# Kernel optimization log

Measured on AMD Instinct MI355X. Metric: run time of the kernel, lower is better.

Reference implementation:

```python
import jax, jax.numpy as jnp
import numpy as np

K = 7          # kernel_size
G = 16         # group_number
C = 256        # channel
R = 4          # reduction_ratio
BN_EPS = 1e-3  # keras BatchNormalization default epsilon


def setup_inputs() -> dict:
    key = jax.random.key(0)
    ks = jax.random.split(key, 8)
    B, H, W = 2, 64, 64
    Cr = C // R
    x = jax.random.normal(ks[0], (B, H, W, C), dtype=jnp.float32)
    # kernel_gen params: 1x1 conv (C->C/r), BN, ReLU, 1x1 conv (C/r -> K*K*G)
    w1 = jax.random.normal(ks[1], (C, Cr), dtype=jnp.float32) * (1.0 / np.sqrt(C))
    b1 = jnp.zeros((Cr,), dtype=jnp.float32)
    gamma = jnp.ones((Cr,), dtype=jnp.float32) + 0.1 * jax.random.normal(ks[2], (Cr,), dtype=jnp.float32)
    beta = 0.1 * jax.random.normal(ks[3], (Cr,), dtype=jnp.float32)
    mu = 0.1 * jax.random.normal(ks[4], (Cr,), dtype=jnp.float32)
    var = jnp.ones((Cr,), dtype=jnp.float32) + 0.05 * jax.random.uniform(ks[5], (Cr,), dtype=jnp.float32)
    w2 = jax.random.normal(ks[6], (Cr, K * K * G), dtype=jnp.float32) * (1.0 / np.sqrt(Cr))
    b2 = jnp.zeros((K * K * G,), dtype=jnp.float32)
    return {"x": x, "w1": w1, "b1": b1, "gamma": gamma, "beta": beta,
            "mu": mu, "var": var, "w2": w2, "b2": b2}


def reference(x, w1, b1, gamma, beta, mu, var, w2, b2):
    B, H, W, _ = x.shape
    # stride == 1 -> stride_layer is identity; kernel_input = x
    # kernel_gen: 1x1 conv -> BN (inference) -> ReLU -> 1x1 conv
    t = jnp.einsum('bhwc,cd->bhwd', x, w1) + b1
    t = gamma * (t - mu) * jax.lax.rsqrt(var + BN_EPS) + beta
    t = jax.nn.relu(t)
    kern = jnp.einsum('bhwd,dk->bhwk', t, w2) + b2            # (B,H,W,K*K*G)
    kern = kern.reshape(B, H, W, K * K, 1, G)                  # (B,H,W,KK,1,G)
    # tf.image.extract_patches SAME, stride 1 -> pad K//2 each side, zeros
    pad = K // 2
    xp = jnp.pad(x, ((0, 0), (pad, pad), (pad, pad), (0, 0)))
    # patch layout matches TF: (kh, kw) outer, channel inner
    patches = jnp.stack(
        [xp[:, i:i + H, j:j + W, :] for i in range(K) for j in range(K)],
        axis=3)                                                # (B,H,W,KK,C)
    patches = patches.reshape(B, H, W, K * K, C // G, G)
    out = jnp.sum(kern * patches, axis=3)                      # (B,H,W,C/G,G)
    out = out.reshape(B, H, W, C)
    return out, kern
```

## Files before the change

### kernel.cpp

```cpp
#include <hip/hip_runtime.h>


typedef __attribute__((ext_vector_type(8))) short short8;
typedef __attribute__((ext_vector_type(4))) float f32x4;

#define OUT_ELEMS 2097152
#define W2S_OFF 0
#define W1S_OFF 131072
#define BNS_OFF (131072 + 32768)
#define BNH_OFF (BNS_OFF + 256)

static __device__ __forceinline__ ushort f2bf(float f) {
    union { float f; unsigned u; } v; v.f = f;
    return (ushort)((v.u + 0x7FFFu + ((v.u >> 16) & 1u)) >> 16);
}

__global__ __launch_bounds__(256)
void prep(const float* __restrict__ w1, const float* __restrict__ w2,
          const float* __restrict__ b1, const float* __restrict__ gamma_,
          const float* __restrict__ beta_, const float* __restrict__ mu_,
          const float* __restrict__ var_, char* __restrict__ base)
{
    const int g = blockIdx.x * 256 + threadIdx.x;
    ushort* w2s = (ushort*)(base + W2S_OFF);
    ushort* w1s = (ushort*)(base + W1S_OFF);
    float*  bns = (float*)(base + BNS_OFF);
    float*  bnh = (float*)(base + BNH_OFF);
    if (g < 50176) {
        const int e = g & 7, lane = (g >> 3) & 63, kgks = g >> 9;
        const int kg = kgks >> 1, ks = kgks & 1;
        const int n = kg * 16 + (lane & 15);
        const int k = ks * 32 + ((lane >> 4) << 3) + e;
        w2s[g] = f2bf(w2[k * 784 + n]);
    } else if (g < 66560) {
        const int e2 = g - 50176;
        const int e = e2 & 7, lane = (e2 >> 3) & 63, ntks = e2 >> 9;
        const int nt = ntks >> 3, ks = ntks & 7;
        const int n = nt * 16 + (lane & 15);
        const int k = ks * 32 + ((lane >> 4) << 3) + e;
        w1s[e2] = f2bf(w1[k * 64 + n]);
    } else if (g < 66624) {
        const int d = g - 66560;
        const float s = gamma_[d] * rsqrtf(var_[d] + 1e-3f);
        bns[d] = s;
        bnh[d] = beta_[d] + (b1[d] - mu_[d]) * s;
    }
}

#define FMA4(A, K, X) \
    A.x = fmaf(K.x, X.x, A.x); A.y = fmaf(K.y, X.y, A.y); \
    A.z = fmaf(K.z, X.z, A.z); A.w = fmaf(K.w, X.w, A.w);

__global__ __launch_bounds__(256)
void invol_fused(const float* __restrict__ x, const char* __restrict__ base,
                 const float* __restrict__ b2, float* __restrict__ kern_out,
                 float* __restrict__ out)
{
    __shared__ __align__(16) union {
        struct { ushort xb[2048]; ushort tb[1024]; } s;
        float kl[6272];
    } u;

    const ushort* w2s = (const ushort*)(base + W2S_OFF);
    const ushort* w1s = (const ushort*)(base + W1S_OFF);
    const float*  bns = (const float*)(base + BNS_OFF);
    const float*  bnh = (const float*)(base + BNH_OFF);

    const int tid  = threadIdx.x;
    const int lane = tid & 63;
    const int wv   = tid >> 6;
    const int bid  = blockIdx.x;
    const int pb   = ((bid & 7) << 10) + ((bid >> 3) << 3);
    const int b  = pb >> 12;
    const int h  = (pb >> 6) & 63;
    const int w0 = pb & 63;

#pragma unroll
    for (int i = 0; i < 2; ++i) {
        const int f4 = tid + 256 * i;
        const int px = f4 >> 6;
        const int c0 = (f4 & 63) * 4;
        const float4 v = *(const float4*)(x + (size_t)(pb + px) * 256 + c0);
        ushort4 hh;
        hh.x = f2bf(v.x); hh.y = f2bf(v.y); hh.z = f2bf(v.z); hh.w = f2bf(v.w);
        const int byte = ((px << 9) + (c0 << 1)) ^ ((px & 7) << 4);
        *(ushort4*)((char*)u.s.xb + byte) = hh;
    }
    __syncthreads();

    const int qlane = lane >> 4;
    const int mrow  = lane & 15;
    const int apx   = mrow & 7;
    const int aswz  = (apx & 7) << 4;

    f32x4 acc = {0.f, 0.f, 0.f, 0.f};
#pragma unroll
    for (int ks = 0; ks < 8; ++ks) {
        const short8 a = *(const short8*)((const char*)u.s.xb +
                          (((apx << 9) + ((ks * 32 + qlane * 8) << 1)) ^ aswz));
        const short8 bv = *(const short8*)(w1s + ((wv * 8 + ks) * 64 + lane) * 8);
        acc = __builtin_amdgcn_mfma_f32_16x16x32_bf16(a, bv, acc, 0, 0, 0);
    }
    if (qlane < 2) {
        const int col = wv * 16 + mrow;
        const float s = bns[col], sh = bnh[col];
#pragma unroll
        for (int r = 0; r < 4; ++r) {
            const int row = qlane * 4 + r;
            const float tv = fmaxf(fmaf(acc[r], s, sh), 0.f);
            const int byte = ((row << 7) + (col << 1)) ^ ((row & 7) << 4);
            *(ushort*)((char*)u.s.tb + byte) = f2bf(tv);
        }
    }
    __syncthreads();

    const short8 a0 = *(const short8*)((const char*)u.s.tb +
                        (((apx << 7) + (qlane << 4)) ^ aswz));
    const short8 a1 = *(const short8*)((const char*)u.s.tb +
                        (((apx << 7) + 64 + (qlane << 4)) ^ aswz));
    __syncthreads();

    for (int kg = wv; kg < 49; kg += 4) {
        const short8 bv0 = *(const short8*)(w2s + (size_t)((kg * 2 + 0) * 64 + lane) * 8);
        const short8 bv1 = *(const short8*)(w2s + (size_t)((kg * 2 + 1) * 64 + lane) * 8);
        f32x4 c = {0.f, 0.f, 0.f, 0.f};
        c = __builtin_amdgcn_mfma_f32_16x16x32_bf16(a0, bv0, c, 0, 0, 0);
        c = __builtin_amdgcn_mfma_f32_16x16x32_bf16(a1, bv1, c, 0, 0, 0);
        if (qlane < 2) {
            const int n = kg * 16 + mrow;
            const float bias = b2[n];
#pragma unroll
            for (int r = 0; r < 4; ++r) {
                const int row = qlane * 4 + r;
                const float val = c[r] + bias;
                kern_out[(size_t)(pb + row) * 784 + n] = val;
                u.kl[row * 784 + n] = val;
            }
        }
    }
    __syncthreads();

    const int c0  = lane * 4;
    const int g0  = c0 & 15;
    const int w0w = w0 + wv * 2;
    const float* xbase = x + ((size_t)b << 20);

    float msk[8]; int colc[8];
#pragma unroll
    for (int j = 0; j < 8; ++j) {
        const int cw = w0w + j - 3;
        msk[j]  = ((unsigned)cw < 64u) ? 1.0f : 0.0f;
        colc[j] = (min(max(cw, 0), 63) << 8) + c0;
    }

    float4 acc4[2];
    acc4[0] = make_float4(0.f, 0.f, 0.f, 0.f);
    acc4[1] = make_float4(0.f, 0.f, 0.f, 0.f);

#pragma unroll
    for (int kh = 0; kh < 7; ++kh) {
        const int hh = h + kh - 3;
        if ((unsigned)hh < 64u) {
            const float* xr = xbase + ((size_t)hh << 14);
            float4 xv[8];
#pragma unroll
            for (int j = 0; j < 8; ++j) {
                xv[j] = *(const float4*)(xr + colc[j]);
                xv[j].x *= msk[j]; xv[j].y *= msk[j];
                xv[j].z *= msk[j]; xv[j].w *= msk[j];
            }
#pragma unroll
            for (int p = 0; p < 2; ++p) {
                const float* kr = u.kl + (wv * 2 + p) * 784 + kh * 112 + g0;
#pragma unroll
                for (int kw = 0; kw < 7; ++kw) {
                    const float4 kv = *(const float4*)(kr + kw * 16);
                    FMA4(acc4[p], kv, xv[p + kw]);
                }
            }
        }
    }
#pragma unroll
    for (int p = 0; p < 2; ++p)
        *(float4*)(out + (size_t)(pb + wv * 2 + p) * 256 + c0) = acc4[p];
}

extern "C" void kernel_launch(void* const* d_in, const int* in_sizes, int n_in,
                              void* d_out, int out_size, void* d_ws, size_t ws_size,
                              hipStream_t stream)
{
    const float* x      = (const float*)d_in[0];
    const float* w1     = (const float*)d_in[1];
    const float* b1     = (const float*)d_in[2];
    const float* gamma_ = (const float*)d_in[3];
    const float* beta_  = (const float*)d_in[4];
    const float* mu_    = (const float*)d_in[5];
    const float* var_   = (const float*)d_in[6];
    const float* w2     = (const float*)d_in[7];
    const float* b2     = (const float*)d_in[8];

    float* out  = (float*)d_out;
    float* kern = out + OUT_ELEMS;
    char*  base = (char*)d_ws;

    prep<<<261, 256, 0, stream>>>(w1, w2, b1, gamma_, beta_, mu_, var_, base);
    invol_fused<<<1024, 256, 0, stream>>>(x, base, b2, kern, out);
}
```

Measured before the change: 101.5 us.

## Process 16 pixels per block with 512 threads to fill MFMA rows

Each block now handles 16 pixels instead of 8 and runs 512 threads, so the 16-row MFMA tiles in both 1x1-conv GEMMs are fully used rather than half wasted. The grid is halved, w2 tiles are read once per 16 pixels, and one barrier is dropped by giving the t tile its own shared buffer. The row-boundary branch in the involution loop becomes a clamped load times a mask, which makes the loop branch-free at the cost of extra loads at the image edges. Shared memory per block roughly doubles, which may lower the number of resident blocks.

Measured after the change: 97.91 us. 3.5% less time.

```diff
diff --git a/kernel.cpp b/kernel.cpp
--- a/kernel.cpp
+++ b/kernel.cpp
@@ -51,15 +51,16 @@
     A.x = fmaf(K.x, X.x, A.x); A.y = fmaf(K.y, X.y, A.y); \
     A.z = fmaf(K.z, X.z, A.z); A.w = fmaf(K.w, X.w, A.w);
 
-__global__ __launch_bounds__(256)
+__global__ __launch_bounds__(512, 4)
 void invol_fused(const float* __restrict__ x, const char* __restrict__ base,
                  const float* __restrict__ b2, float* __restrict__ kern_out,
                  float* __restrict__ out)
 {
     __shared__ __align__(16) union {
-        struct { ushort xb[2048]; ushort tb[1024]; } s;
-        float kl[6272];
+        ushort xb[4096];
+        float  kl[12544];
     } u;
+    __shared__ __align__(16) ushort tb[1024];
 
     const ushort* w2s = (const ushort*)(base + W2S_OFF);
     const ushort* w1s = (const ushort*)(base + W1S_OFF);
@@ -70,38 +71,37 @@
     const int lane = tid & 63;
     const int wv   = tid >> 6;
     const int bid  = blockIdx.x;
-    const int pb   = ((bid & 7) << 10) + ((bid >> 3) << 3);
+    const int pb   = ((bid & 7) << 10) + ((bid >> 3) << 4);
     const int b  = pb >> 12;
     const int h  = (pb >> 6) & 63;
     const int w0 = pb & 63;
 
 #pragma unroll
     for (int i = 0; i < 2; ++i) {
-        const int f4 = tid + 256 * i;
+        const int f4 = tid + 512 * i;
         const int px = f4 >> 6;
         const int c0 = (f4 & 63) * 4;
         const float4 v = *(const float4*)(x + (size_t)(pb + px) * 256 + c0);
         ushort4 hh;
         hh.x = f2bf(v.x); hh.y = f2bf(v.y); hh.z = f2bf(v.z); hh.w = f2bf(v.w);
         const int byte = ((px << 9) + (c0 << 1)) ^ ((px & 7) << 4);
-        *(ushort4*)((char*)u.s.xb + byte) = hh;
+        *(ushort4*)((char*)u.xb + byte) = hh;
     }
     __syncthreads();
 
     const int qlane = lane >> 4;
     const int mrow  = lane & 15;
-    const int apx   = mrow & 7;
-    const int aswz  = (apx & 7) << 4;
-
-    f32x4 acc = {0.f, 0.f, 0.f, 0.f};
-#pragma unroll
-    for (int ks = 0; ks < 8; ++ks) {
-        const short8 a = *(const short8*)((const char*)u.s.xb +
-                          (((apx << 9) + ((ks * 32 + qlane * 8) << 1)) ^ aswz));
-        const short8 bv = *(const short8*)(w1s + ((wv * 8 + ks) * 64 + lane) * 8);
-        acc = __builtin_amdgcn_mfma_f32_16x16x32_bf16(a, bv, acc, 0, 0, 0);
-    }
-    if (qlane < 2) {
+    const int aswz  = (mrow & 7) << 4;
+
+    if (wv < 4) {
+        f32x4 acc = {0.f, 0.f, 0.f, 0.f};
+#pragma unroll
+        for (int ks = 0; ks < 8; ++ks) {
+            const short8 a = *(const short8*)((const char*)u.xb +
+                              (((mrow << 9) + ((ks * 32 + qlane * 8) << 1)) ^ aswz));
+            const short8 bv = *(const short8*)(w1s + ((wv * 8 + ks) * 64 + lane) * 8);
+            acc = __builtin_amdgcn_mfma_f32_16x16x32_bf16(a, bv, acc, 0, 0, 0);
+        }
         const int col = wv * 16 + mrow;
         const float s = bns[col], sh = bnh[col];
 #pragma unroll
@@ -109,33 +109,30 @@
             const int row = qlane * 4 + r;
             const float tv = fmaxf(fmaf(acc[r], s, sh), 0.f);
             const int byte = ((row << 7) + (col << 1)) ^ ((row & 7) << 4);
-            *(ushort*)((char*)u.s.tb + byte) = f2bf(tv);
+            *(ushort*)((char*)tb + byte) = f2bf(tv);
         }
     }
     __syncthreads();
 
-    const short8 a0 = *(const short8*)((const char*)u.s.tb +
-                        (((apx << 7) + (qlane << 4)) ^ aswz));
-    const short8 a1 = *(const short8*)((const char*)u.s.tb +
-                        (((apx << 7) + 64 + (qlane << 4)) ^ aswz));
-    __syncthreads();
-
-    for (int kg = wv; kg < 49; kg += 4) {
+    const short8 a0 = *(const short8*)((const char*)tb +
+                        (((mrow << 7) + (qlane << 4)) ^ aswz));
+    const short8 a1 = *(const short8*)((const char*)tb +
+                        (((mrow << 7) + 64 + (qlane << 4)) ^ aswz));
+
+    for (int kg = wv; kg < 49; kg += 8) {
         const short8 bv0 = *(const short8*)(w2s + (size_t)((kg * 2 + 0) * 64 + lane) * 8);
         const short8 bv1 = *(const short8*)(w2s + (size_t)((kg * 2 + 1) * 64 + lane) * 8);
         f32x4 c = {0.f, 0.f, 0.f, 0.f};
         c = __builtin_amdgcn_mfma_f32_16x16x32_bf16(a0, bv0, c, 0, 0, 0);
         c = __builtin_amdgcn_mfma_f32_16x16x32_bf16(a1, bv1, c, 0, 0, 0);
-        if (qlane < 2) {
-            const int n = kg * 16 + mrow;
-            const float bias = b2[n];
-#pragma unroll
-            for (int r = 0; r < 4; ++r) {
-                const int row = qlane * 4 + r;
-                const float val = c[r] + bias;
-                kern_out[(size_t)(pb + row) * 784 + n] = val;
-                u.kl[row * 784 + n] = val;
-            }
+        const int n = kg * 16 + mrow;
+        const float bias = b2[n];
+#pragma unroll
+        for (int r = 0; r < 4; ++r) {
+            const int row = qlane * 4 + r;
+            const float val = c[r] + bias;
+            kern_out[(size_t)(pb + row) * 784 + n] = val;
+            u.kl[row * 784 + n] = val;
         }
     }
     __syncthreads();
@@ -160,23 +157,23 @@
 #pragma unroll
     for (int kh = 0; kh < 7; ++kh) {
         const int hh = h + kh - 3;
-        if ((unsigned)hh < 64u) {
-            const float* xr = xbase + ((size_t)hh << 14);
-            float4 xv[8];
-#pragma unroll
-            for (int j = 0; j < 8; ++j) {
-                xv[j] = *(const float4*)(xr + colc[j]);
-                xv[j].x *= msk[j]; xv[j].y *= msk[j];
-                xv[j].z *= msk[j]; xv[j].w *= msk[j];
-            }
-#pragma unroll
-            for (int p = 0; p < 2; ++p) {
-                const float* kr = u.kl + (wv * 2 + p) * 784 + kh * 112 + g0;
-#pragma unroll
-                for (int kw = 0; kw < 7; ++kw) {
-                    const float4 kv = *(const float4*)(kr + kw * 16);
-                    FMA4(acc4[p], kv, xv[p + kw]);
-                }
+        const float rm = ((unsigned)hh < 64u) ? 1.0f : 0.0f;
+        const int hc = min(max(hh, 0), 63);
+        const float* xr = xbase + ((size_t)hc << 14);
+        float4 xv[8];
+#pragma unroll
+        for (int j = 0; j < 8; ++j) {
+            xv[j] = *(const float4*)(xr + colc[j]);
+            const float s = msk[j] * rm;
+            xv[j].x *= s; xv[j].y *= s; xv[j].z *= s; xv[j].w *= s;
+        }
+#pragma unroll
+        for (int p = 0; p < 2; ++p) {
+            const float* kr = u.kl + (wv * 2 + p) * 784 + kh * 112 + g0;
+#pragma unroll
+            for (int kw = 0; kw < 7; ++kw) {
+                const float4 kv = *(const float4*)(kr + kw * 16);
+                FMA4(acc4[p], kv, xv[p + kw]);
             }
         }
     }
@@ -204,5 +201,5 @@
     char*  base = (char*)d_ws;
 
     prep<<<261, 256, 0, stream>>>(w1, w2, b1, gamma_, beta_, mu_, var_, base);
-    invol_fused<<<1024, 256, 0, stream>>>(x, base, b2, kern, out);
-}
+    invol_fused<<<512, 512, 0, stream>>>(x, base, b2, kern, out);
+}
```
